# Kernel optimization log

Measured on AMD Instinct MI355X. Metric: run time of the kernel, lower is better.

Reference implementation:

```python
import jax, jax.numpy as jnp
import numpy as np

S = 128           # seq_len
B = 256           # input_bits (bits per token, also neurons per head)
H = 16            # num_heads
NB = 12           # n_bits_per_neuron -> LUT size 2^12
PB = 7            # relative-position bits = ceil(log2(max_seq_len))
HEAD_IN = 2 * B + PB   # concat(query, key, rel_pos_bits) = 519
THRESH = H // 2


def setup_inputs() -> dict:
    key = jax.random.key(0)
    k1, k2, k3 = jax.random.split(key, 3)
    tokens = jax.random.randint(k1, (S, B), 0, 2, dtype=jnp.int32)           # binary token bits
    memory = jax.random.normal(k2, (H, B, 2 ** NB), dtype=jnp.float32)       # RAM LUT contents per head/neuron
    connections = jax.random.randint(k3, (H, B, NB), 0, HEAD_IN, dtype=jnp.int32)  # per-neuron input-bit wiring
    return {"tokens": tokens, "memory": memory, "connections": connections}


def reference(tokens, memory, connections):
    idx = jnp.arange(S)
    rel = idx[:, None] - idx[None, :]                         # [S,S] i - j
    mask = (rel >= 0).astype(jnp.int32)                        # causal mask (j <= i)
    relc = jnp.clip(rel, 0, S - 1)
    # relative-distance binary encoding, LSB first: [S,S,PB]
    pos_bits = ((relc[..., None] >> jnp.arange(PB)) & 1).astype(jnp.int32)
    q = jnp.broadcast_to(tokens[:, None, :], (S, S, B))
    k = jnp.broadcast_to(tokens[None, :, :], (S, S, B))
    head_in = jnp.concatenate([q, k, pos_bits], axis=-1)       # [S,S,HEAD_IN]
    # RAM address per (query i, key j, head h, neuron n): pack NB wired bits, LSB first
    addr = jnp.zeros((S, S, H, B), dtype=jnp.int32)
    for b in range(NB):  # tiny fixed loop over bit planes, fully vectorized over S,S,H,B
        addr = addr + (head_in[..., connections[:, :, b]] << b)
    # LUT gather: memory[h, n, addr] -> [S,S,H,B]
    h_idx = jnp.arange(H)[:, None]
    n_idx = jnp.arange(B)[None, :]
    vals = memory[h_idx, n_idx, addr]
    bits = (vals > 0.0).astype(jnp.int32)                      # RAM neuron output bit
    # XOR accumulation over attended keys == masked sum mod 2: [S,H,B]
    head_res = jnp.sum(bits * mask[:, :, None, None], axis=1) % 2
    # majority vote across heads per bit
    ones_count = jnp.sum(head_res, axis=1)                     # [S,B]
    return (ones_count > THRESH).astype(jnp.int32)
```

## Files before the change

### kernel.cpp

```cpp
#include <hip/hip_runtime.h>
#include <hip/hip_bf16.h>


#define S 128
#define B 256
#define H 16
#define NB 12

__device__ __forceinline__ unsigned sig(unsigned x) {
    return x ^ ((x >> 3) & 0x70u) ^ ((x >> 6) & 0x70u);
}

__global__ __launch_bounds__(1024) void softram_kernel(
    const int* __restrict__ tokens,
    const float* __restrict__ memory,
    const int* __restrict__ connections,
    int* __restrict__ out)
{
    const int n    = blockIdx.x;
    const int tid  = threadIdx.x;
    const int h    = tid >> 6;
    const int lane = tid & 63;

    __shared__ unsigned char  bytetab[H * 4096];
    __shared__ unsigned int   tokT[8][S];
    __shared__ unsigned short aqsig[H][S];
    __shared__ unsigned short aksig[H][S];
    __shared__ unsigned short apsig[H][S];
    __shared__ int            conns[H][NB];
    __shared__ unsigned int   parts[H][4];

    {
        int i = tid >> 3, w = tid & 7;
        const int4* tp = (const int4*)tokens;
        unsigned v = 0;
        #pragma unroll
        for (int u = 0; u < 8; ++u) {
            int4 x = tp[i * 64 + w * 8 + u];
            v |= (unsigned)(x.x & 1) << (4 * u + 0);
            v |= (unsigned)(x.y & 1) << (4 * u + 1);
            v |= (unsigned)(x.z & 1) << (4 * u + 2);
            v |= (unsigned)(x.w & 1) << (4 * u + 3);
        }
        tokT[w][i] = v;
    }
    if (tid < H * NB) {
        int hh = tid / NB, b = tid - hh * NB;
        conns[hh][b] = connections[hh * (B * NB) + n * NB + b];
    }
    __syncthreads();

    const float4* mrow = (const float4*)(memory + ((size_t)(h * 256 + n) << 12));
    float4 va[16];
    #pragma unroll
    for (int t = 0; t < 16; ++t) va[t] = mrow[lane + 64 * t];

    unsigned qmask = 0, kmask = 0, pmask = 0;
    #pragma unroll
    for (int b = 0; b < NB; ++b) {
        int c = conns[h][b];
        qmask |= (unsigned)(c < 256) << b;
        kmask |= (unsigned)(c >= 256 && c < 512) << b;
        pmask |= (unsigned)(c >= 512) << b;
    }

    #pragma unroll
    for (int e = 0; e < 2; ++e) {
        int ii = lane + 64 * e;
        unsigned aq = 0, ak = 0, ap = 0;
        #pragma unroll
        for (int b = 0; b < NB; ++b) {
            int c = conns[h][b];
            if (c < 256) {
                aq |= ((tokT[c >> 5][ii] >> (c & 31)) & 1u) << b;
            } else if (c < 512) {
                int c2 = c - 256;
                ak |= ((tokT[c2 >> 5][ii] >> (c2 & 31)) & 1u) << b;
            } else {
                ap |= ((unsigned)(ii >> (c - 512)) & 1u) << b;
            }
        }
        aqsig[h][ii] = (unsigned short)sig(aq);
        aksig[h][ii] = (unsigned short)sig(ak);
        apsig[h][ii] = (unsigned short)sig(ap);
    }

    unsigned char* __restrict__ bt = &bytetab[h << 12];
    #pragma unroll
    for (int t = 0; t < 16; ++t) {
        float4 v = va[t];
        unsigned p = 4u * (unsigned)(lane + 64 * t);
        unsigned w = (unsigned)(v.x > 0.f)
                   | ((unsigned)(v.y > 0.f) << 8)
                   | ((unsigned)(v.z > 0.f) << 16)
                   | ((unsigned)(v.w > 0.f) << 24);
        *(unsigned*)&bt[sig(p)] = w;
    }

    unsigned long long rlo = 0, rhi = 0;

    if (pmask == 0) {
        int qb = __popc(qmask), kb = __popc(kmask);
        bool sideQ = (qb <= kb);
        unsigned smask = sideQ ? qmask : kmask;
        int m = sideQ ? qb : kb;
        unsigned spread = 0;
        {
            unsigned k = (unsigned)lane;
            #pragma unroll
            for (int b = 0; b < NB; ++b) {
                if ((smask >> b) & 1u) { spread |= (k & 1u) << b; k >>= 1; }
            }
        }
        const unsigned spv = sig(spread);
        const int lim = 1 << m;
        const bool lv = (lane < lim);
        const unsigned long long vmask =
            (lim >= 64) ? ~0ull : ((1ull << lim) - 1ull);

        if (sideQ) {
            unsigned acc = 0;
            for (int s8 = 0; s8 < 16; ++s8) {
                uint4 uq = *(const uint4*)&aqsig[h][s8 * 8];
                uint4 uk = *(const uint4*)&aksig[h][s8 * 8];
                #pragma unroll
                for (int t = 0; t < 8; ++t) {
                    int j = s8 * 8 + t;
                    unsigned cwk = ((const unsigned*)&uk)[t >> 1];
                    unsigned cwq = ((const unsigned*)&uq)[t >> 1];
                    unsigned akv = (cwk >> ((t & 1) * 16)) & 0xffffu;
                    unsigned aqv = (cwq >> ((t & 1) * 16)) & 0xffffu;
                    acc ^= bt[akv ^ spv];
                    unsigned long long accB = __ballot((acc & 1u) != 0u);
                    unsigned long long mm   = __ballot(lv && (spv == aqv));
                    unsigned long long bit  = ((accB & mm & vmask) != 0ull);
                    if (j < 64) rlo |= bit << j; else rhi |= bit << (j - 64);
                }
            }
        } else {
            unsigned c = 0;
            for (int s8 = 0; s8 < 16; ++s8) {
                uint4 uq = *(const uint4*)&aqsig[h][s8 * 8];
                uint4 uk = *(const uint4*)&aksig[h][s8 * 8];
                #pragma unroll
                for (int t = 0; t < 8; ++t) {
                    int i = s8 * 8 + t;
                    unsigned cwk = ((const unsigned*)&uk)[t >> 1];
                    unsigned cwq = ((const unsigned*)&uq)[t >> 1];
                    unsigned akv = (cwk >> ((t & 1) * 16)) & 0xffffu;
                    unsigned aqv = (cwq >> ((t & 1) * 16)) & 0xffffu;
                    c ^= (unsigned)(lv && (spv == akv));
                    unsigned sb = bt[aqv ^ spv];
                    unsigned long long mb = __ballot((c & sb & 1u) != 0u);
                    unsigned long long bit = (unsigned long long)
                        (__popcll(mb & vmask) & 1ull);
                    if (i < 64) rlo |= bit << i; else rhi |= bit << (i - 64);
                }
            }
        }
    } else {
        const unsigned ak0 = aksig[h][lane];
        const unsigned ak1 = aksig[h][lane + 64];
        for (int s8 = 0; s8 < 16; ++s8) {
            uint4 uq = *(const uint4*)&aqsig[h][s8 * 8];
            #pragma unroll
            for (int t = 0; t < 8; ++t) {
                int i = s8 * 8 + t;
                unsigned cwq = ((const unsigned*)&uq)[t >> 1];
                unsigned aqv = (cwq >> ((t & 1) * 16)) & 0xffffu;
                unsigned ap0 = apsig[h][(i - lane) & 127];
                unsigned v0  = bt[aqv ^ ak0 ^ ap0];
                unsigned long long m0 = __ballot((v0 & 1u) != 0u);
                unsigned long long pre0 =
                    (i >= 63) ? ~0ull : ((2ull << i) - 1ull);
                unsigned cnt = (unsigned)__popcll(m0 & pre0);
                if (i >= 64) {
                    unsigned ap1 = apsig[h][(i - lane - 64) & 127];
                    unsigned v1  = bt[aqv ^ ak1 ^ ap1];
                    unsigned long long m1 = __ballot((v1 & 1u) != 0u);
                    unsigned long long pre1 =
                        (i >= 127) ? ~0ull : ((2ull << (i - 64)) - 1ull);
                    cnt += (unsigned)__popcll(m1 & pre1);
                }
                unsigned long long bit = cnt & 1u;
                if (i < 64) rlo |= bit << i; else rhi |= bit << (i - 64);
            }
        }
    }

    if (lane == 0) {
        parts[h][0] = (unsigned)rlo;
        parts[h][1] = (unsigned)(rlo >> 32);
        parts[h][2] = (unsigned)rhi;
        parts[h][3] = (unsigned)(rhi >> 32);
    }
    __syncthreads();

    if (tid < S) {
        int i = tid, tot = 0;
        #pragma unroll
        for (int hh = 0; hh < H; ++hh)
            tot += (parts[hh][i >> 5] >> (i & 31)) & 1;
        out[i * B + n] = (tot > (H / 2)) ? 1 : 0;
    }
}

extern "C" void kernel_launch(void* const* d_in, const int* in_sizes, int n_in,
                              void* d_out, int out_size, void* d_ws, size_t ws_size,
                              hipStream_t stream) {
    const int*   tokens      = (const int*)d_in[0];
    const float* memory      = (const float*)d_in[1];
    const int*   connections = (const int*)d_in[2];
    int*         out         = (int*)d_out;
    (void)in_sizes; (void)n_in; (void)out_size; (void)d_ws; (void)ws_size;

    softram_kernel<<<B, 1024, 0, stream>>>(tokens, memory, connections, out);
}
```

Before: 112.8 us.

## Prepack LUT signs into bitmasks in a separate kernel and use bit-table lookups

Adds a pre-pass kernel that turns each float LUT entry into a sign bit via wave ballots, writes 64-bit masks to workspace, and packs the token bits once. The main kernel then loads only 512 bytes of bits per head-neuron instead of 16 KB of floats. It swaps the 64 KB shared byte table for a 512-byte-per-head word table with a new bank-swizzling address code. Lookups become a word load plus a shift. The cost is an extra kernel launch and a global round trip through the workspace, while the memory is still read in full once.

```diff
diff --git a/kernel.cpp b/kernel.cpp
--- a/kernel.cpp
+++ b/kernel.cpp
@@ -7,13 +7,58 @@
 #define H 16
 #define NB 12
 
-__device__ __forceinline__ unsigned sig(unsigned x) {
-    return x ^ ((x >> 3) & 0x70u) ^ ((x >> 6) & 0x70u);
-}
-
-__global__ __launch_bounds__(1024) void softram_kernel(
+__global__ __launch_bounds__(256) void softram_pack(
+    const float* __restrict__ memory,
     const int* __restrict__ tokens,
-    const float* __restrict__ memory,
+    unsigned long long* __restrict__ lut64,
+    unsigned int* __restrict__ tokpack)
+{
+    const int bx = blockIdx.x, tid = threadIdx.x;
+    const int w = tid >> 6, lane = tid & 63;
+    const float4* mp = (const float4*)memory;
+    #pragma unroll
+    for (int it = 0; it < 16; ++it) {
+        int chunk = bx * 64 + w * 16 + it;
+        float4 v = mp[chunk * 64 + lane];
+        unsigned long long b0 = __ballot(v.x > 0.f);
+        unsigned long long b1 = __ballot(v.y > 0.f);
+        unsigned long long b2 = __ballot(v.z > 0.f);
+        unsigned long long b3 = __ballot(v.w > 0.f);
+        unsigned long long sel = b0;
+        sel = (lane == 1) ? b1 : sel;
+        sel = (lane == 2) ? b2 : sel;
+        sel = (lane == 3) ? b3 : sel;
+        if (lane < 4) lut64[chunk * 4 + lane] = sel;
+    }
+    if (bx == 0) {
+        #pragma unroll
+        for (int q = 0; q < 4; ++q) {
+            int e = tid + (q << 8);
+            int i = e >> 3, ww = e & 7;
+            const int4* tp = (const int4*)tokens;
+            unsigned vv = 0;
+            #pragma unroll
+            for (int u = 0; u < 8; ++u) {
+                int4 x = tp[i * 64 + ww * 8 + u];
+                vv |= (unsigned)(x.x & 1) << (4 * u + 0);
+                vv |= (unsigned)(x.y & 1) << (4 * u + 1);
+                vv |= (unsigned)(x.z & 1) << (4 * u + 2);
+                vv |= (unsigned)(x.w & 1) << (4 * u + 3);
+            }
+            tokpack[ww * 128 + i] = vv;
+        }
+    }
+}
+
+__device__ __forceinline__ unsigned codef(unsigned r) {
+    unsigned cw = ((r >> 7) & 1u) | ((r & 3u) << 1) | (((r >> 8) & 15u) << 3);
+    cw ^= ((cw >> 5) & 3u) << 1;
+    return cw | (((r >> 2) & 31u) << 7);
+}
+
+__global__ __launch_bounds__(1024) void softram_main(
+    const unsigned long long* __restrict__ lut64,
+    const unsigned int* __restrict__ tokpack,
     const int* __restrict__ connections,
     int* __restrict__ out)
 {
@@ -22,38 +67,28 @@
     const int h    = tid >> 6;
     const int lane = tid & 63;
 
-    __shared__ unsigned char  bytetab[H * 4096];
+    __shared__ unsigned int   lutw[H][128];
     __shared__ unsigned int   tokT[8][S];
-    __shared__ unsigned short aqsig[H][S];
-    __shared__ unsigned short aksig[H][S];
-    __shared__ unsigned short apsig[H][S];
+    __shared__ unsigned short aqc[H][S];
+    __shared__ unsigned short akc[H][S];
+    __shared__ unsigned short apc[H][S];
     __shared__ int            conns[H][NB];
     __shared__ unsigned int   parts[H][4];
 
-    {
-        int i = tid >> 3, w = tid & 7;
-        const int4* tp = (const int4*)tokens;
-        unsigned v = 0;
-        #pragma unroll
-        for (int u = 0; u < 8; ++u) {
-            int4 x = tp[i * 64 + w * 8 + u];
-            v |= (unsigned)(x.x & 1) << (4 * u + 0);
-            v |= (unsigned)(x.y & 1) << (4 * u + 1);
-            v |= (unsigned)(x.z & 1) << (4 * u + 2);
-            v |= (unsigned)(x.w & 1) << (4 * u + 3);
-        }
-        tokT[w][i] = v;
-    }
+    tokT[tid >> 7][tid & 127] = tokpack[tid];
     if (tid < H * NB) {
         int hh = tid / NB, b = tid - hh * NB;
         conns[hh][b] = connections[hh * (B * NB) + n * NB + b];
     }
     __syncthreads();
 
-    const float4* mrow = (const float4*)(memory + ((size_t)(h * 256 + n) << 12));
-    float4 va[16];
-    #pragma unroll
-    for (int t = 0; t < 16; ++t) va[t] = mrow[lane + 64 * t];
+    {
+        unsigned long long wrow = lut64[(size_t)((h << 8) | n) * 64 + lane];
+        unsigned wpos = (unsigned)(2 * lane);
+        wpos ^= ((wpos >> 5) & 3u) << 1;
+        lutw[h][wpos]     = (unsigned)wrow;
+        lutw[h][wpos + 1] = (unsigned)(wrow >> 32);
+    }
 
     unsigned qmask = 0, kmask = 0, pmask = 0;
     #pragma unroll
@@ -80,23 +115,12 @@
                 ap |= ((unsigned)(ii >> (c - 512)) & 1u) << b;
             }
         }
-        aqsig[h][ii] = (unsigned short)sig(aq);
-        aksig[h][ii] = (unsigned short)sig(ak);
-        apsig[h][ii] = (unsigned short)sig(ap);
-    }
-
-    unsigned char* __restrict__ bt = &bytetab[h << 12];
-    #pragma unroll
-    for (int t = 0; t < 16; ++t) {
-        float4 v = va[t];
-        unsigned p = 4u * (unsigned)(lane + 64 * t);
-        unsigned w = (unsigned)(v.x > 0.f)
-                   | ((unsigned)(v.y > 0.f) << 8)
-                   | ((unsigned)(v.z > 0.f) << 16)
-                   | ((unsigned)(v.w > 0.f) << 24);
-        *(unsigned*)&bt[sig(p)] = w;
-    }
-
+        aqc[h][ii] = (unsigned short)codef(aq);
+        akc[h][ii] = (unsigned short)codef(ak);
+        apc[h][ii] = (unsigned short)codef(ap);
+    }
+
+    const unsigned* __restrict__ lrow = &lutw[h][0];
     unsigned long long rlo = 0, rhi = 0;
 
     if (pmask == 0) {
@@ -112,7 +136,7 @@
                 if ((smask >> b) & 1u) { spread |= (k & 1u) << b; k >>= 1; }
             }
         }
-        const unsigned spv = sig(spread);
+        const unsigned spv = codef(spread);
         const int lim = 1 << m;
         const bool lv = (lane < lim);
         const unsigned long long vmask =
@@ -121,8 +145,8 @@
         if (sideQ) {
             unsigned acc = 0;
             for (int s8 = 0; s8 < 16; ++s8) {
-                uint4 uq = *(const uint4*)&aqsig[h][s8 * 8];
-                uint4 uk = *(const uint4*)&aksig[h][s8 * 8];
+                uint4 uq = *(const uint4*)&aqc[h][s8 * 8];
+                uint4 uk = *(const uint4*)&akc[h][s8 * 8];
                 #pragma unroll
                 for (int t = 0; t < 8; ++t) {
                     int j = s8 * 8 + t;
@@ -130,7 +154,8 @@
                     unsigned cwq = ((const unsigned*)&uq)[t >> 1];
                     unsigned akv = (cwk >> ((t & 1) * 16)) & 0xffffu;
                     unsigned aqv = (cwq >> ((t & 1) * 16)) & 0xffffu;
-                    acc ^= bt[akv ^ spv];
+                    unsigned vt = akv ^ spv;
+                    acc ^= lrow[vt & 127] >> (vt >> 7);
                     unsigned long long accB = __ballot((acc & 1u) != 0u);
                     unsigned long long mm   = __ballot(lv && (spv == aqv));
                     unsigned long long bit  = ((accB & mm & vmask) != 0ull);
@@ -140,8 +165,8 @@
         } else {
             unsigned c = 0;
             for (int s8 = 0; s8 < 16; ++s8) {
-                uint4 uq = *(const uint4*)&aqsig[h][s8 * 8];
-                uint4 uk = *(const uint4*)&aksig[h][s8 * 8];
+                uint4 uq = *(const uint4*)&aqc[h][s8 * 8];
+                uint4 uk = *(const uint4*)&akc[h][s8 * 8];
                 #pragma unroll
                 for (int t = 0; t < 8; ++t) {
                     int i = s8 * 8 + t;
@@ -150,7 +175,8 @@
                     unsigned akv = (cwk >> ((t & 1) * 16)) & 0xffffu;
                     unsigned aqv = (cwq >> ((t & 1) * 16)) & 0xffffu;
                     c ^= (unsigned)(lv && (spv == akv));
-                    unsigned sb = bt[aqv ^ spv];
+                    unsigned vt = aqv ^ spv;
+                    unsigned sb = lrow[vt & 127] >> (vt >> 7);
                     unsigned long long mb = __ballot((c & sb & 1u) != 0u);
                     unsigned long long bit = (unsigned long long)
                         (__popcll(mb & vmask) & 1ull);
@@ -159,24 +185,26 @@
             }
         }
     } else {
-        const unsigned ak0 = aksig[h][lane];
-        const unsigned ak1 = aksig[h][lane + 64];
+        const unsigned ak0 = akc[h][lane];
+        const unsigned ak1 = akc[h][lane + 64];
         for (int s8 = 0; s8 < 16; ++s8) {
-            uint4 uq = *(const uint4*)&aqsig[h][s8 * 8];
+            uint4 uq = *(const uint4*)&aqc[h][s8 * 8];
             #pragma unroll
             for (int t = 0; t < 8; ++t) {
                 int i = s8 * 8 + t;
                 unsigned cwq = ((const unsigned*)&uq)[t >> 1];
                 unsigned aqv = (cwq >> ((t & 1) * 16)) & 0xffffu;
-                unsigned ap0 = apsig[h][(i - lane) & 127];
-                unsigned v0  = bt[aqv ^ ak0 ^ ap0];
+                unsigned ap0 = apc[h][(i - lane) & 127];
+                unsigned t0  = aqv ^ ak0 ^ ap0;
+                unsigned v0  = lrow[t0 & 127] >> (t0 >> 7);
                 unsigned long long m0 = __ballot((v0 & 1u) != 0u);
                 unsigned long long pre0 =
                     (i >= 63) ? ~0ull : ((2ull << i) - 1ull);
                 unsigned cnt = (unsigned)__popcll(m0 & pre0);
                 if (i >= 64) {
-                    unsigned ap1 = apsig[h][(i - lane - 64) & 127];
-                    unsigned v1  = bt[aqv ^ ak1 ^ ap1];
+                    unsigned ap1 = apc[h][(i - lane - 64) & 127];
+                    unsigned t1  = aqv ^ ak1 ^ ap1;
+                    unsigned v1  = lrow[t1 & 127] >> (t1 >> 7);
                     unsigned long long m1 = __ballot((v1 & 1u) != 0u);
                     unsigned long long pre1 =
                         (i >= 127) ? ~0ull : ((2ull << (i - 64)) - 1ull);
@@ -212,7 +240,11 @@
     const float* memory      = (const float*)d_in[1];
     const int*   connections = (const int*)d_in[2];
     int*         out         = (int*)d_out;
-    (void)in_sizes; (void)n_in; (void)out_size; (void)d_ws; (void)ws_size;
-
-    softram_kernel<<<B, 1024, 0, stream>>>(tokens, memory, connections, out);
-}
+    (void)in_sizes; (void)n_in; (void)out_size; (void)ws_size;
+
+    unsigned long long* lut64   = (unsigned long long*)d_ws;
+    unsigned int*       tokpack = (unsigned int*)((char*)d_ws + (2u << 20));
+
+    softram_pack<<<1024, 256, 0, stream>>>(memory, tokens, lut64, tokpack);
+    softram_main<<<B, 1024, 0, stream>>>(lut64, tokpack, connections, out);
+}
```

After: 129.7 us. 1.15x slower.

## Bit-pack LUTs and replace per-query loops with sub-table transpose and XOR prefix scans

Applied to the files above, without the earlier changes.

The LUT is now compressed to a 4096-bit packed table per head, built with wave ballots instead of a byte table. When no position bits are wired, each head precomputes a 64x64 sub-table over the query/key address split and answers every query with a wave-wide XOR prefix scan. This replaces the 128-step sequential ballot loop. The position-bit path is restructured into per-lane loops over relative distance, reading the packed bits. This cuts LDS footprint and serial wave steps, but adds shuffle scans and assumes a 6-bit split of the address bits between query and key.

```diff
diff --git a/kernel.cpp b/kernel.cpp
--- a/kernel.cpp
+++ b/kernel.cpp
@@ -7,8 +7,22 @@
 #define H 16
 #define NB 12
 
-__device__ __forceinline__ unsigned sig(unsigned x) {
-    return x ^ ((x >> 3) & 0x70u) ^ ((x >> 6) & 0x70u);
+__device__ __forceinline__ unsigned pdep12(unsigned val, unsigned mask) {
+    unsigned r = 0; int t = 0;
+    #pragma unroll
+    for (int b = 0; b < NB; ++b) {
+        if ((mask >> b) & 1u) { r |= ((val >> t) & 1u) << b; ++t; }
+    }
+    return r;
+}
+
+__device__ __forceinline__ unsigned scan_xor32(unsigned x, int lane) {
+    #pragma unroll
+    for (int off = 1; off < 64; off <<= 1) {
+        unsigned y = __shfl_up(x, off, 64);
+        x ^= (lane >= off) ? y : 0u;
+    }
+    return x;
 }
 
 __global__ __launch_bounds__(1024) void softram_kernel(
@@ -22,13 +36,13 @@
     const int h    = tid >> 6;
     const int lane = tid & 63;
 
-    __shared__ unsigned char  bytetab[H * 4096];
-    __shared__ unsigned int   tokT[8][S];
-    __shared__ unsigned short aqsig[H][S];
-    __shared__ unsigned short aksig[H][S];
-    __shared__ unsigned short apsig[H][S];
-    __shared__ int            conns[H][NB];
-    __shared__ unsigned int   parts[H][4];
+    __shared__ unsigned long long packA[H * 64];
+    __shared__ unsigned long long trowA[H * 64];
+    __shared__ unsigned int       tokT[8][S];
+    __shared__ unsigned short     aksv[H * 128];
+    __shared__ unsigned short     apsv[H * 128];
+    __shared__ int                conns[H][NB];
+    __shared__ unsigned int       parts[H][4];
 
     {
         int i = tid >> 3, w = tid & 7;
@@ -50,10 +64,21 @@
     }
     __syncthreads();
 
-    const float4* mrow = (const float4*)(memory + ((size_t)(h * 256 + n) << 12));
-    float4 va[16];
-    #pragma unroll
-    for (int t = 0; t < 16; ++t) va[t] = mrow[lane + 64 * t];
+    const float* row = memory + ((size_t)(h * 256 + n) << 12);
+    unsigned long long pk = 0;
+    #pragma unroll
+    for (int co = 0; co < 8; ++co) {
+        float v[8];
+        #pragma unroll
+        for (int ci = 0; ci < 8; ++ci) v[ci] = row[(co * 8 + ci) * 64 + lane];
+        #pragma unroll
+        for (int ci = 0; ci < 8; ++ci) {
+            unsigned long long bal = __ballot(v[ci] > 0.0f);
+            if (lane == co * 8 + ci) pk = bal;
+        }
+    }
+    packA[h * 64 + lane] = pk;
+    const unsigned* pk32 = (const unsigned*)&packA[h * 64];
 
     unsigned qmask = 0, kmask = 0, pmask = 0;
     #pragma unroll
@@ -63,136 +88,125 @@
         kmask |= (unsigned)(c >= 256 && c < 512) << b;
         pmask |= (unsigned)(c >= 512) << b;
     }
-
-    #pragma unroll
-    for (int e = 0; e < 2; ++e) {
-        int ii = lane + 64 * e;
-        unsigned aq = 0, ak = 0, ap = 0;
-        #pragma unroll
-        for (int b = 0; b < NB; ++b) {
-            int c = conns[h][b];
-            if (c < 256) {
-                aq |= ((tokT[c >> 5][ii] >> (c & 31)) & 1u) << b;
-            } else if (c < 512) {
-                int c2 = c - 256;
-                ak |= ((tokT[c2 >> 5][ii] >> (c2 & 31)) & 1u) << b;
-            } else {
-                ap |= ((unsigned)(ii >> (c - 512)) & 1u) << b;
-            }
-        }
-        aqsig[h][ii] = (unsigned short)sig(aq);
-        aksig[h][ii] = (unsigned short)sig(ak);
-        apsig[h][ii] = (unsigned short)sig(ap);
-    }
-
-    unsigned char* __restrict__ bt = &bytetab[h << 12];
-    #pragma unroll
-    for (int t = 0; t < 16; ++t) {
-        float4 v = va[t];
-        unsigned p = 4u * (unsigned)(lane + 64 * t);
-        unsigned w = (unsigned)(v.x > 0.f)
-                   | ((unsigned)(v.y > 0.f) << 8)
-                   | ((unsigned)(v.z > 0.f) << 16)
-                   | ((unsigned)(v.w > 0.f) << 24);
-        *(unsigned*)&bt[sig(p)] = w;
-    }
-
-    unsigned long long rlo = 0, rhi = 0;
+    unsigned qi0 = 0, qi1 = 0, ki0 = 0, ki1 = 0;
+    unsigned aqv0 = 0, aqv1 = 0, akv0 = 0, akv1 = 0, apv0 = 0, apv1 = 0;
+    int qc = 0, kc = 0;
+    #pragma unroll
+    for (int b = 0; b < NB; ++b) {
+        int c = conns[h][b];
+        if (c < 256) {
+            unsigned b0 = (tokT[c >> 5][lane]      >> (c & 31)) & 1u;
+            unsigned b1 = (tokT[c >> 5][lane + 64] >> (c & 31)) & 1u;
+            qi0 |= b0 << qc; qi1 |= b1 << qc;
+            aqv0 |= b0 << b;  aqv1 |= b1 << b;  ++qc;
+        } else if (c < 512) {
+            int c2 = c - 256;
+            unsigned b0 = (tokT[c2 >> 5][lane]      >> (c2 & 31)) & 1u;
+            unsigned b1 = (tokT[c2 >> 5][lane + 64] >> (c2 & 31)) & 1u;
+            ki0 |= b0 << kc; ki1 |= b1 << kc;
+            akv0 |= b0 << b;  akv1 |= b1 << b;  ++kc;
+        } else {
+            int t = c - 512;
+            apv0 |= (((unsigned)lane >> t) & 1u) << b;
+            apv1 |= ((((unsigned)lane + 64u) >> t) & 1u) << b;
+        }
+    }
+    aksv[h * 128 + lane]      = (unsigned short)akv0;
+    aksv[h * 128 + lane + 64] = (unsigned short)akv1;
+    apsv[h * 128 + lane]      = (unsigned short)apv0;
+    apsv[h * 128 + lane + 64] = (unsigned short)apv1;
+
+    const int qb = __popc(qmask), kb = __popc(kmask);
+    unsigned rb0 = 0, rb1 = 0;
 
     if (pmask == 0) {
-        int qb = __popc(qmask), kb = __popc(kmask);
-        bool sideQ = (qb <= kb);
-        unsigned smask = sideQ ? qmask : kmask;
-        int m = sideQ ? qb : kb;
-        unsigned spread = 0;
-        {
-            unsigned k = (unsigned)lane;
-            #pragma unroll
-            for (int b = 0; b < NB; ++b) {
-                if ((smask >> b) & 1u) { spread |= (k & 1u) << b; k >>= 1; }
-            }
-        }
-        const unsigned spv = sig(spread);
-        const int lim = 1 << m;
-        const bool lv = (lane < lim);
-        const unsigned long long vmask =
-            (lim >= 64) ? ~0ull : ((1ull << lim) - 1ull);
-
-        if (sideQ) {
-            unsigned acc = 0;
-            for (int s8 = 0; s8 < 16; ++s8) {
-                uint4 uq = *(const uint4*)&aqsig[h][s8 * 8];
-                uint4 uk = *(const uint4*)&aksig[h][s8 * 8];
-                #pragma unroll
-                for (int t = 0; t < 8; ++t) {
-                    int j = s8 * 8 + t;
-                    unsigned cwk = ((const unsigned*)&uk)[t >> 1];
-                    unsigned cwq = ((const unsigned*)&uq)[t >> 1];
-                    unsigned akv = (cwk >> ((t & 1) * 16)) & 0xffffu;
-                    unsigned aqv = (cwq >> ((t & 1) * 16)) & 0xffffu;
-                    acc ^= bt[akv ^ spv];
-                    unsigned long long accB = __ballot((acc & 1u) != 0u);
-                    unsigned long long mm   = __ballot(lv && (spv == aqv));
-                    unsigned long long bit  = ((accB & mm & vmask) != 0ull);
-                    if (j < 64) rlo |= bit << j; else rhi |= bit << (j - 64);
-                }
-            }
+        const bool pathA = (qb <= 6);
+        const unsigned maskI = pathA ? qmask : kmask;
+        const unsigned maskO = pathA ? kmask : qmask;
+        const int bi = pathA ? qb : kb;
+        const unsigned im = (1u << bi) - 1u;
+        const unsigned spl = pdep12((unsigned)lane & im, maskI)
+                           | pdep12((unsigned)lane >> bi, maskO);
+        const unsigned spE = pdep12((unsigned)lane << (6 - bi), maskO);
+
+        unsigned long long tr = 0;
+        #pragma unroll
+        for (int e = 0; e < 64; ++e) {
+            unsigned spe = __builtin_amdgcn_readlane(spE, e);
+            unsigned x = spe ^ spl;
+            unsigned w = pk32[x >> 5];
+            unsigned long long bal = __ballot(((w >> (x & 31)) & 1u) != 0u);
+            if (lane == e) tr = bal;
+        }
+        trowA[h * 64 + lane] = tr;
+
+        const unsigned long long* tw = &trowA[h * 64];
+        const int olb = 6 - bi;
+        const unsigned olm = (1u << olb) - 1u;
+
+        if (pathA) {
+            const unsigned long long wm =
+                (bi == 6) ? ~0ull : ((1ull << (1u << bi)) - 1ull);
+            unsigned long long w0 = tw[ki0 >> olb];
+            unsigned long long T0 = (w0 >> ((ki0 & olm) << bi)) & wm;
+            unsigned long long w1 = tw[ki1 >> olb];
+            unsigned long long T1 = (w1 >> ((ki1 & olm) << bi)) & wm;
+            unsigned t0lo = scan_xor32((unsigned)T0, lane);
+            unsigned t0hi = scan_xor32((unsigned)(T0 >> 32), lane);
+            unsigned tlo63 = __shfl(t0lo, 63, 64);
+            unsigned thi63 = __shfl(t0hi, 63, 64);
+            unsigned t1lo = scan_xor32((unsigned)T1, lane) ^ tlo63;
+            unsigned t1hi = scan_xor32((unsigned)(T1 >> 32), lane) ^ thi63;
+            unsigned long long W0 = ((unsigned long long)t0hi << 32) | t0lo;
+            unsigned long long W1 = ((unsigned long long)t1hi << 32) | t1lo;
+            rb0 = (unsigned)(W0 >> qi0) & 1u;
+            rb1 = (unsigned)(W1 >> qi1) & 1u;
         } else {
-            unsigned c = 0;
-            for (int s8 = 0; s8 < 16; ++s8) {
-                uint4 uq = *(const uint4*)&aqsig[h][s8 * 8];
-                uint4 uk = *(const uint4*)&aksig[h][s8 * 8];
-                #pragma unroll
-                for (int t = 0; t < 8; ++t) {
-                    int i = s8 * 8 + t;
-                    unsigned cwk = ((const unsigned*)&uk)[t >> 1];
-                    unsigned cwq = ((const unsigned*)&uq)[t >> 1];
-                    unsigned akv = (cwk >> ((t & 1) * 16)) & 0xffffu;
-                    unsigned aqv = (cwq >> ((t & 1) * 16)) & 0xffffu;
-                    c ^= (unsigned)(lv && (spv == akv));
-                    unsigned sb = bt[aqv ^ spv];
-                    unsigned long long mb = __ballot((c & sb & 1u) != 0u);
-                    unsigned long long bit = (unsigned long long)
-                        (__popcll(mb & vmask) & 1ull);
-                    if (i < 64) rlo |= bit << i; else rhi |= bit << (i - 64);
-                }
-            }
+            const unsigned sm = (unsigned)((1ull << (1u << bi)) - 1ull);
+            unsigned C0 = scan_xor32(1u << ki0, lane);
+            unsigned c63 = __shfl(C0, 63, 64);
+            unsigned C1 = scan_xor32(1u << ki1, lane) ^ c63;
+            unsigned long long w0 = tw[qi0 >> olb];
+            unsigned Sl0 = (unsigned)(w0 >> ((qi0 & olm) << bi)) & sm;
+            unsigned long long w1 = tw[qi1 >> olb];
+            unsigned Sl1 = (unsigned)(w1 >> ((qi1 & olm) << bi)) & sm;
+            rb0 = (unsigned)__popc(Sl0 & C0) & 1u;
+            rb1 = (unsigned)__popc(Sl1 & C1) & 1u;
         }
     } else {
-        const unsigned ak0 = aksig[h][lane];
-        const unsigned ak1 = aksig[h][lane + 64];
-        for (int s8 = 0; s8 < 16; ++s8) {
-            uint4 uq = *(const uint4*)&aqsig[h][s8 * 8];
-            #pragma unroll
-            for (int t = 0; t < 8; ++t) {
-                int i = s8 * 8 + t;
-                unsigned cwq = ((const unsigned*)&uq)[t >> 1];
-                unsigned aqv = (cwq >> ((t & 1) * 16)) & 0xffffu;
-                unsigned ap0 = apsig[h][(i - lane) & 127];
-                unsigned v0  = bt[aqv ^ ak0 ^ ap0];
-                unsigned long long m0 = __ballot((v0 & 1u) != 0u);
-                unsigned long long pre0 =
-                    (i >= 63) ? ~0ull : ((2ull << i) - 1ull);
-                unsigned cnt = (unsigned)__popcll(m0 & pre0);
-                if (i >= 64) {
-                    unsigned ap1 = apsig[h][(i - lane - 64) & 127];
-                    unsigned v1  = bt[aqv ^ ak1 ^ ap1];
-                    unsigned long long m1 = __ballot((v1 & 1u) != 0u);
-                    unsigned long long pre1 =
-                        (i >= 127) ? ~0ull : ((2ull << (i - 64)) - 1ull);
-                    cnt += (unsigned)__popcll(m1 & pre1);
-                }
-                unsigned long long bit = cnt & 1u;
-                if (i < 64) rlo |= bit << i; else rhi |= bit << (i - 64);
-            }
-        }
-    }
-
+        const unsigned short* aks = &aksv[h * 128];
+        const unsigned short* aps = &apsv[h * 128];
+        unsigned acc0 = 0, acc1 = 0;
+        #pragma unroll 8
+        for (int d = 0; d < 64; ++d) {
+            unsigned apd = aps[d];
+            unsigned ak0 = aks[(lane - d) & 127];
+            unsigned x0 = aqv0 ^ ak0 ^ apd;
+            unsigned bit0 = (pk32[x0 >> 5] >> (x0 & 31)) & 1u;
+            acc0 ^= (lane >= d) ? bit0 : 0u;
+            unsigned ak1 = aks[(lane + 64 - d) & 127];
+            unsigned x1 = aqv1 ^ ak1 ^ apd;
+            acc1 ^= (pk32[x1 >> 5] >> (x1 & 31)) & 1u;
+        }
+        #pragma unroll 8
+        for (int d = 64; d < 128; ++d) {
+            unsigned apd = aps[d];
+            unsigned ak1 = aks[(lane + 64 - d) & 127];
+            unsigned x1 = aqv1 ^ ak1 ^ apd;
+            unsigned bit1 = (pk32[x1 >> 5] >> (x1 & 31)) & 1u;
+            acc1 ^= (lane + 64 >= d) ? bit1 : 0u;
+        }
+        rb0 = acc0 & 1u;
+        rb1 = acc1 & 1u;
+    }
+
+    unsigned long long blo = __ballot(rb0 != 0u);
+    unsigned long long bhi = __ballot(rb1 != 0u);
     if (lane == 0) {
-        parts[h][0] = (unsigned)rlo;
-        parts[h][1] = (unsigned)(rlo >> 32);
-        parts[h][2] = (unsigned)rhi;
-        parts[h][3] = (unsigned)(rhi >> 32);
+        parts[h][0] = (unsigned)blo;
+        parts[h][1] = (unsigned)(blo >> 32);
+        parts[h][2] = (unsigned)bhi;
+        parts[h][3] = (unsigned)(bhi >> 32);
     }
     __syncthreads();
 
```

Result: slower. 125.0 us (+10.8%).
